# Kernel tuning notes

Hardware: AMD Instinct MI355X
Metric: run time of the kernel (lower is better)

The kernel has to match this reference:

```python
import jax, jax.numpy as jnp
import numpy as np

B, N, DIN, DOUT = 64, 128, 64, 64
EDGE_P = 0.05  # adjacency density


def setup_inputs() -> dict:
    key = jax.random.key(0)
    k1, k2, k3, k4 = jax.random.split(key, 4)
    # 2D tuple features: X[b, i, k, :] is the feature of tuple (i, k) in graph b
    X = jax.random.normal(k1, (B, N, N, DIN), dtype=jnp.float32)
    # sparse adjacency realized densely as 0/1 floats (PygHO 'DD' masked mode)
    A = (jax.random.uniform(k2, (B, N, N)) < EDGE_P).astype(jnp.float32)
    # tuplewise MLP (default mlp={} -> single Linear indim->outdim)
    W = (jax.random.normal(k3, (DIN, DOUT), dtype=jnp.float32) / np.sqrt(DIN)).astype(jnp.float32)
    b = jnp.zeros((DOUT,), dtype=jnp.float32)
    return {"X": X, "A": A, "W": W, "b": b}


def reference(X, A, W, b):
    # tuplewiseapply(MLP): dense linear on the last (feature) dim of every tuple
    tX = jnp.einsum('bikd,de->bike', X, W) + b          # [B, N, N, DOUT]
    # OpMessagePassingOnSubg2D, aggr='sum':
    # out[b, i, j, :] = sum_k tX[b, i, k, :] * A[b, k, j]
    out = jnp.einsum('bike,bkj->bije', tX, A)           # [B, N, N, DOUT]
    return out
```

## Files before the change

### kernel.cpp

```cpp
#include <hip/hip_runtime.h>

#define NGRAPH 64
#define NN 128
#define DI 64
#define DO 64

typedef __attribute__((ext_vector_type(8))) short short8;
typedef __attribute__((ext_vector_type(4))) short short4v;
typedef __attribute__((ext_vector_type(4))) float f32x4;

#define OFF_COLSUM (2u * 1024u * 1024u)
#define OFF_WTHI   (OFF_COLSUM + 32u * 1024u)
#define OFF_WTLO   (OFF_WTHI + 8u * 1024u)
#define WS_NEED    (OFF_WTLO + 8u * 1024u)

__device__ __forceinline__ unsigned short f2bf_rn(float f) {
    unsigned int u = __float_as_uint(f);
    u += 0x7FFFu + ((u >> 16) & 1u);
    return (unsigned short)(u >> 16);
}
__device__ __forceinline__ float bf2f(unsigned short h) {
    return __uint_as_float(((unsigned int)h) << 16);
}

__global__ __launch_bounds__(256) void prep_adj(const float* __restrict__ A,
                                                short* __restrict__ AT,
                                                float* __restrict__ colsum) {
    __shared__ float csp[2][NN];
    const int b  = blockIdx.x;
    const int j  = threadIdx.x & 127;
    const int kh = threadIdx.x >> 7;
    const float* Ab = A + (size_t)b * NN * NN;
    short* ATr = AT + (size_t)b * NN * NN + (size_t)j * NN + kh * 64;
    float s = 0.f;
    for (int kc = 0; kc < 8; ++kc) {
        short8 pk;
        #pragma unroll
        for (int u = 0; u < 8; ++u) {
            float a = Ab[(size_t)(kh * 64 + kc * 8 + u) * NN + j];
            s += a;
            pk[u] = (short)f2bf_rn(a);
        }
        *(short8*)(ATr + kc * 8) = pk;
    }
    csp[kh][j] = s;
    __syncthreads();
    if (kh == 0) colsum[b * NN + j] = csp[0][j] + csp[1][j];
}

__global__ void prep_w(const float* __restrict__ W,
                       short* __restrict__ WThi, short* __restrict__ WTlo) {
    const int t = threadIdx.x;
    for (int m = 0; m < 16; ++m) {
        int idx = m * 256 + t;
        int e = idx >> 6, d = idx & 63;
        float x = W[d * 64 + e];
        unsigned short h = f2bf_rn(x);
        unsigned short lo = f2bf_rn(x - bf2f(h));
        WThi[idx] = (short)h;
        WTlo[idx] = (short)lo;
    }
}

#define TSTR 136

__global__ __launch_bounds__(256, 3)
void ngnn_main(const float* __restrict__ X,
               const short* __restrict__ AT,
               const float* __restrict__ bias,
               const float* __restrict__ colsum,
               const short* __restrict__ WThi,
               const short* __restrict__ WTlo,
               float* __restrict__ out) {
    __shared__ short tXThi[DO][TSTR];
    __shared__ short tXTlo[DO][TSTR];

    const int tid = threadIdx.x;
    const int w   = tid >> 6;
    const int l   = tid & 63;
    const int lm  = l & 15;
    const int lg  = l >> 4;
    const int b   = blockIdx.x >> 7;

    const float* Xb = X + (size_t)blockIdx.x * (NN * DI);

    short8 wfh[4][2], wfl[4][2];
    #pragma unroll
    for (int nt = 0; nt < 4; ++nt)
        #pragma unroll
        for (int ks = 0; ks < 2; ++ks) {
            int off = (nt * 16 + lm) * DI + ks * 32 + lg * 8;
            wfh[nt][ks] = *(const short8*)(WThi + off);
            wfl[nt][ks] = *(const short8*)(WTlo + off);
        }

    #pragma unroll
    for (int mt = 0; mt < 2; ++mt) {
        const int krow = (w * 2 + mt) * 16 + lm;
        const float* xr = Xb + (size_t)krow * DI;
        short8 xh[2], xl[2];
        #pragma unroll
        for (int ks = 0; ks < 2; ++ks) {
            float4 a = ((const float4*)xr)[ks * 8 + lg * 2];
            float4 c4 = ((const float4*)xr)[ks * 8 + lg * 2 + 1];
            float v[8] = {a.x, a.y, a.z, a.w, c4.x, c4.y, c4.z, c4.w};
            #pragma unroll
            for (int u = 0; u < 8; ++u) {
                unsigned short h = f2bf_rn(v[u]);
                xh[ks][u] = (short)h;
                xl[ks][u] = (short)f2bf_rn(v[u] - bf2f(h));
            }
        }
        #pragma unroll
        for (int nt = 0; nt < 4; ++nt) {
            f32x4 c = {0.f, 0.f, 0.f, 0.f};
            #pragma unroll
            for (int ks = 0; ks < 2; ++ks) {
                c = __builtin_amdgcn_mfma_f32_16x16x32_bf16(xh[ks], wfh[nt][ks], c, 0, 0, 0);
                c = __builtin_amdgcn_mfma_f32_16x16x32_bf16(xh[ks], wfl[nt][ks], c, 0, 0, 0);
                c = __builtin_amdgcn_mfma_f32_16x16x32_bf16(xl[ks], wfh[nt][ks], c, 0, 0, 0);
            }
            const int e  = nt * 16 + lm;
            const int kb = (w * 2 + mt) * 16 + lg * 4;
            short4v h4, l4;
            #pragma unroll
            for (int r = 0; r < 4; ++r) {
                unsigned short h = f2bf_rn(c[r]);
                h4[r] = (short)h;
                l4[r] = (short)f2bf_rn(c[r] - bf2f(h));
            }
            *(short4v*)&tXThi[e][kb] = h4;
            *(short4v*)&tXTlo[e][kb] = l4;
        }
    }
    __syncthreads();

    const short* ATb = AT + (size_t)b * NN * NN;
    f32x4 acc[8];
    #pragma unroll
    for (int nt = 0; nt < 8; ++nt) acc[nt] = (f32x4){0.f, 0.f, 0.f, 0.f};

    #pragma unroll
    for (int ks = 0; ks < 4; ++ks) {
        short8 ah = *(const short8*)&tXThi[w * 16 + lm][ks * 32 + lg * 8];
        short8 al = *(const short8*)&tXTlo[w * 16 + lm][ks * 32 + lg * 8];
        #pragma unroll
        for (int nt = 0; nt < 8; ++nt) {
            short8 bf = *(const short8*)(ATb + (size_t)(nt * 16 + lm) * NN + ks * 32 + lg * 8);
            acc[nt] = __builtin_amdgcn_mfma_f32_16x16x32_bf16(ah, bf, acc[nt], 0, 0, 0);
            acc[nt] = __builtin_amdgcn_mfma_f32_16x16x32_bf16(al, bf, acc[nt], 0, 0, 0);
        }
    }

    const int e0 = w * 16 + lg * 4;
    const float4 bv = *(const float4*)(bias + e0);
    float* outb = out + (size_t)blockIdx.x * (NN * DO);
    #pragma unroll
    for (int nt = 0; nt < 8; ++nt) {
        const int j = nt * 16 + lm;
        const float cs = colsum[b * NN + j];
        float4 o;
        o.x = acc[nt][0] + bv.x * cs;
        o.y = acc[nt][1] + bv.y * cs;
        o.z = acc[nt][2] + bv.z * cs;
        o.w = acc[nt][3] + bv.w * cs;
        *(float4*)(outb + (size_t)j * DO + e0) = o;
    }
}

__global__ __launch_bounds__(256, 3)
void fallback_dense(const float* __restrict__ X,
                    const float* __restrict__ A,
                    const float* __restrict__ W,
                    const float* __restrict__ bias,
                    float* __restrict__ out) {
    __shared__ float tXs[NN][DO + 4];
    __shared__ float Ws[DI][DO];
    __shared__ float bs[DO];
    const int tid = threadIdx.x;
    const int bb = blockIdx.x >> 7;

    {
        const float4* Wv = (const float4*)W;
        float4* Wsv = (float4*)&Ws[0][0];
        #pragma unroll
        for (int t = 0; t < 4; ++t) Wsv[tid + 256 * t] = Wv[tid + 256 * t];
        if (tid < DO) bs[tid] = bias[tid];
    }
    __syncthreads();
    {
        const int k = tid & 127;
        const int e0 = (tid >> 7) * 32;
        const float4* Xv = (const float4*)(X + (size_t)blockIdx.x * (NN * DI) + (size_t)k * DI);
        float acc[32];
        #pragma unroll
        for (int q = 0; q < 32; ++q) acc[q] = 0.f;
        for (int dq = 0; dq < DI / 4; ++dq) {
            float4 xv = Xv[dq];
            const float xs[4] = {xv.x, xv.y, xv.z, xv.w};
            #pragma unroll
            for (int s = 0; s < 4; ++s) {
                const float4* wrow = (const float4*)&Ws[dq * 4 + s][e0];
                #pragma unroll
                for (int q = 0; q < 8; ++q) {
                    float4 wv = wrow[q];
                    acc[q * 4 + 0] = fmaf(xs[s], wv.x, acc[q * 4 + 0]);
                    acc[q * 4 + 1] = fmaf(xs[s], wv.y, acc[q * 4 + 1]);
                    acc[q * 4 + 2] = fmaf(xs[s], wv.z, acc[q * 4 + 2]);
                    acc[q * 4 + 3] = fmaf(xs[s], wv.w, acc[q * 4 + 3]);
                }
            }
        }
        float4* trow = (float4*)&tXs[k][e0];
        #pragma unroll
        for (int q = 0; q < 8; ++q)
            trow[q] = make_float4(acc[q * 4], acc[q * 4 + 1], acc[q * 4 + 2], acc[q * 4 + 3]);
    }
    __syncthreads();
    {
        const int lane = tid & 63;
        const int g = tid >> 6;
        const float bl = bs[lane];
        float* outb = out + (size_t)blockIdx.x * (NN * DO);
        for (int jj = 0; jj < 32; ++jj) {
            const int j = g * 32 + jj;
            const float* Acol = A + (size_t)bb * NN * NN + j;
            float acc2 = 0.f, cs = 0.f;
            for (int k = 0; k < NN; ++k) {
                float a = Acol[(size_t)k * NN];
                cs += a;
                acc2 = fmaf(a, tXs[k][lane], acc2);
            }
            outb[(size_t)j * DO + lane] = acc2 + bl * cs;
        }
    }
}

extern "C" void kernel_launch(void* const* d_in, const int* in_sizes, int n_in,
                              void* d_out, int out_size, void* d_ws, size_t ws_size,
                              hipStream_t stream) {
    const float* X    = (const float*)d_in[0];
    const float* A    = (const float*)d_in[1];
    const float* W    = (const float*)d_in[2];
    const float* bias = (const float*)d_in[3];
    float* out = (float*)d_out;

    if (d_ws != nullptr && ws_size >= WS_NEED) {
        char* ws = (char*)d_ws;
        short* ATp    = (short*)ws;
        float* colsum = (float*)(ws + OFF_COLSUM);
        short* WThi   = (short*)(ws + OFF_WTHI);
        short* WTlo   = (short*)(ws + OFF_WTLO);

        hipLaunchKernelGGL(prep_adj, dim3(NGRAPH), dim3(256), 0, stream, A, ATp, colsum);
        hipLaunchKernelGGL(prep_w, dim3(1), dim3(256), 0, stream, W, WThi, WTlo);
        hipLaunchKernelGGL(ngnn_main, dim3(NGRAPH * NN), dim3(256), 0, stream,
                           X, ATp, bias, colsum, WThi, WTlo, out);
    } else {
        hipLaunchKernelGGL(fallback_dense, dim3(NGRAPH * NN), dim3(256), 0, stream,
                           X, A, W, bias, out);
    }
}
```

Baseline: 570.8 us.

## Prefetch X, adjacency and colsum early; split prep_adj across more blocks

The main kernel now issues all global loads up front (raw X rows, the first adjacency slice, colsum values and bias) so their latency overlaps the first GEMM. W fragments are loaded per output tile rather than all held at once, and the occupancy hint rises from 3 to 4 blocks per CU. prep_adj is split into 4 blocks per graph with 8 k-slices each, giving it more parallelism. The cost is higher register pressure from the prefetched values, which could cause spilling at the tighter launch bound.

```diff
diff --git a/kernel.cpp b/kernel.cpp
--- a/kernel.cpp
+++ b/kernel.cpp
@@ -26,31 +26,40 @@
 __global__ __launch_bounds__(256) void prep_adj(const float* __restrict__ A,
                                                 short* __restrict__ AT,
                                                 float* __restrict__ colsum) {
-    __shared__ float csp[2][NN];
-    const int b  = blockIdx.x;
-    const int j  = threadIdx.x & 127;
-    const int kh = threadIdx.x >> 7;
+    const int b  = blockIdx.x >> 2;
+    const int jq = blockIdx.x & 3;
+    const int jl = threadIdx.x & 31;
+    const int j  = jq * 32 + jl;
+    const int k8 = threadIdx.x >> 5;
+    __shared__ float csp[8][32];
     const float* Ab = A + (size_t)b * NN * NN;
-    short* ATr = AT + (size_t)b * NN * NN + (size_t)j * NN + kh * 64;
+    short* ATr = AT + (size_t)b * NN * NN + (size_t)j * NN + k8 * 16;
     float s = 0.f;
-    for (int kc = 0; kc < 8; ++kc) {
+    #pragma unroll
+    for (int c = 0; c < 2; ++c) {
         short8 pk;
         #pragma unroll
         for (int u = 0; u < 8; ++u) {
-            float a = Ab[(size_t)(kh * 64 + kc * 8 + u) * NN + j];
+            float a = Ab[(size_t)(k8 * 16 + c * 8 + u) * NN + j];
             s += a;
             pk[u] = (short)f2bf_rn(a);
         }
-        *(short8*)(ATr + kc * 8) = pk;
-    }
-    csp[kh][j] = s;
-    __syncthreads();
-    if (kh == 0) colsum[b * NN + j] = csp[0][j] + csp[1][j];
+        *(short8*)(ATr + c * 8) = pk;
+    }
+    csp[k8][jl] = s;
+    __syncthreads();
+    if (k8 == 0) {
+        float t = 0.f;
+        #pragma unroll
+        for (int q = 0; q < 8; ++q) t += csp[q][jl];
+        colsum[b * NN + j] = t;
+    }
 }
 
 __global__ void prep_w(const float* __restrict__ W,
                        short* __restrict__ WThi, short* __restrict__ WTlo) {
     const int t = threadIdx.x;
+    #pragma unroll
     for (int m = 0; m < 16; ++m) {
         int idx = m * 256 + t;
         int e = idx >> 6, d = idx & 63;
@@ -64,7 +73,7 @@
 
 #define TSTR 136
 
-__global__ __launch_bounds__(256, 3)
+__global__ __launch_bounds__(256, 4)
 void ngnn_main(const float* __restrict__ X,
                const short* __restrict__ AT,
                const float* __restrict__ bias,
@@ -82,44 +91,61 @@
     const int lg  = l >> 4;
     const int b   = blockIdx.x >> 7;
 
-    const float* Xb = X + (size_t)blockIdx.x * (NN * DI);
-
-    short8 wfh[4][2], wfl[4][2];
-    #pragma unroll
-    for (int nt = 0; nt < 4; ++nt)
+    const float* Xb  = X + (size_t)blockIdx.x * (NN * DI);
+    const short* ATb = AT + (size_t)b * NN * NN;
+
+    const float4* xr0 = (const float4*)(Xb + (size_t)((w * 2 + 0) * 16 + lm) * DI);
+    const float4* xr1 = (const float4*)(Xb + (size_t)((w * 2 + 1) * 16 + lm) * DI);
+    float4 xraw[8];
+    #pragma unroll
+    for (int ks = 0; ks < 2; ++ks) {
+        xraw[ks * 2 + 0]     = xr0[ks * 8 + lg * 2];
+        xraw[ks * 2 + 1]     = xr0[ks * 8 + lg * 2 + 1];
+        xraw[4 + ks * 2 + 0] = xr1[ks * 8 + lg * 2];
+        xraw[4 + ks * 2 + 1] = xr1[ks * 8 + lg * 2 + 1];
+    }
+    short8 bf0[8];
+    #pragma unroll
+    for (int nt = 0; nt < 8; ++nt)
+        bf0[nt] = *(const short8*)(ATb + (size_t)(nt * 16 + lm) * NN + lg * 8);
+    float csv[8];
+    #pragma unroll
+    for (int nt = 0; nt < 8; ++nt)
+        csv[nt] = colsum[b * NN + nt * 16 + lm];
+    const float4 bv = *(const float4*)(bias + w * 16 + lg * 4);
+
+    short8 xh[2][2], xl[2][2];
+    #pragma unroll
+    for (int mt = 0; mt < 2; ++mt)
         #pragma unroll
         for (int ks = 0; ks < 2; ++ks) {
-            int off = (nt * 16 + lm) * DI + ks * 32 + lg * 8;
-            wfh[nt][ks] = *(const short8*)(WThi + off);
-            wfl[nt][ks] = *(const short8*)(WTlo + off);
-        }
-
-    #pragma unroll
-    for (int mt = 0; mt < 2; ++mt) {
-        const int krow = (w * 2 + mt) * 16 + lm;
-        const float* xr = Xb + (size_t)krow * DI;
-        short8 xh[2], xl[2];
-        #pragma unroll
-        for (int ks = 0; ks < 2; ++ks) {
-            float4 a = ((const float4*)xr)[ks * 8 + lg * 2];
-            float4 c4 = ((const float4*)xr)[ks * 8 + lg * 2 + 1];
+            float4 a  = xraw[mt * 4 + ks * 2];
+            float4 c4 = xraw[mt * 4 + ks * 2 + 1];
             float v[8] = {a.x, a.y, a.z, a.w, c4.x, c4.y, c4.z, c4.w};
             #pragma unroll
             for (int u = 0; u < 8; ++u) {
                 unsigned short h = f2bf_rn(v[u]);
-                xh[ks][u] = (short)h;
-                xl[ks][u] = (short)f2bf_rn(v[u] - bf2f(h));
-            }
-        }
-        #pragma unroll
-        for (int nt = 0; nt < 4; ++nt) {
+                xh[mt][ks][u] = (short)h;
+                xl[mt][ks][u] = (short)f2bf_rn(v[u] - bf2f(h));
+            }
+        }
+
+    const int eo = lm * DI + lg * 8;
+    #pragma unroll
+    for (int nt = 0; nt < 4; ++nt) {
+        const short8 wh0 = *(const short8*)(WThi + nt * 16 * DI + eo);
+        const short8 wh1 = *(const short8*)(WThi + nt * 16 * DI + eo + 32);
+        const short8 wl0 = *(const short8*)(WTlo + nt * 16 * DI + eo);
+        const short8 wl1 = *(const short8*)(WTlo + nt * 16 * DI + eo + 32);
+        #pragma unroll
+        for (int mt = 0; mt < 2; ++mt) {
             f32x4 c = {0.f, 0.f, 0.f, 0.f};
-            #pragma unroll
-            for (int ks = 0; ks < 2; ++ks) {
-                c = __builtin_amdgcn_mfma_f32_16x16x32_bf16(xh[ks], wfh[nt][ks], c, 0, 0, 0);
-                c = __builtin_amdgcn_mfma_f32_16x16x32_bf16(xh[ks], wfl[nt][ks], c, 0, 0, 0);
-                c = __builtin_amdgcn_mfma_f32_16x16x32_bf16(xl[ks], wfh[nt][ks], c, 0, 0, 0);
-            }
+            c = __builtin_amdgcn_mfma_f32_16x16x32_bf16(xh[mt][0], wh0, c, 0, 0, 0);
+            c = __builtin_amdgcn_mfma_f32_16x16x32_bf16(xh[mt][0], wl0, c, 0, 0, 0);
+            c = __builtin_amdgcn_mfma_f32_16x16x32_bf16(xl[mt][0], wh0, c, 0, 0, 0);
+            c = __builtin_amdgcn_mfma_f32_16x16x32_bf16(xh[mt][1], wh1, c, 0, 0, 0);
+            c = __builtin_amdgcn_mfma_f32_16x16x32_bf16(xh[mt][1], wl1, c, 0, 0, 0);
+            c = __builtin_amdgcn_mfma_f32_16x16x32_bf16(xl[mt][1], wh1, c, 0, 0, 0);
             const int e  = nt * 16 + lm;
             const int kb = (w * 2 + mt) * 16 + lg * 4;
             short4v h4, l4;
@@ -135,30 +161,36 @@
     }
     __syncthreads();
 
-    const short* ATb = AT + (size_t)b * NN * NN;
     f32x4 acc[8];
     #pragma unroll
     for (int nt = 0; nt < 8; ++nt) acc[nt] = (f32x4){0.f, 0.f, 0.f, 0.f};
 
     #pragma unroll
     for (int ks = 0; ks < 4; ++ks) {
-        short8 ah = *(const short8*)&tXThi[w * 16 + lm][ks * 32 + lg * 8];
-        short8 al = *(const short8*)&tXTlo[w * 16 + lm][ks * 32 + lg * 8];
+        const short8 ah = *(const short8*)&tXThi[w * 16 + lm][ks * 32 + lg * 8];
+        const short8 al = *(const short8*)&tXTlo[w * 16 + lm][ks * 32 + lg * 8];
+        short8 bfv[8];
+        if (ks == 0) {
+            #pragma unroll
+            for (int nt = 0; nt < 8; ++nt) bfv[nt] = bf0[nt];
+        } else {
+            #pragma unroll
+            for (int nt = 0; nt < 8; ++nt)
+                bfv[nt] = *(const short8*)(ATb + (size_t)(nt * 16 + lm) * NN + ks * 32 + lg * 8);
+        }
         #pragma unroll
         for (int nt = 0; nt < 8; ++nt) {
-            short8 bf = *(const short8*)(ATb + (size_t)(nt * 16 + lm) * NN + ks * 32 + lg * 8);
-            acc[nt] = __builtin_amdgcn_mfma_f32_16x16x32_bf16(ah, bf, acc[nt], 0, 0, 0);
-            acc[nt] = __builtin_amdgcn_mfma_f32_16x16x32_bf16(al, bf, acc[nt], 0, 0, 0);
+            acc[nt] = __builtin_amdgcn_mfma_f32_16x16x32_bf16(ah, bfv[nt], acc[nt], 0, 0, 0);
+            acc[nt] = __builtin_amdgcn_mfma_f32_16x16x32_bf16(al, bfv[nt], acc[nt], 0, 0, 0);
         }
     }
 
     const int e0 = w * 16 + lg * 4;
-    const float4 bv = *(const float4*)(bias + e0);
     float* outb = out + (size_t)blockIdx.x * (NN * DO);
     #pragma unroll
     for (int nt = 0; nt < 8; ++nt) {
         const int j = nt * 16 + lm;
-        const float cs = colsum[b * NN + j];
+        const float cs = csv[nt];
         float4 o;
         o.x = acc[nt][0] + bv.x * cs;
         o.y = acc[nt][1] + bv.y * cs;
@@ -179,7 +211,6 @@
     __shared__ float bs[DO];
     const int tid = threadIdx.x;
     const int bb = blockIdx.x >> 7;
-
     {
         const float4* Wv = (const float4*)W;
         float4* Wsv = (float4*)&Ws[0][0];
@@ -252,7 +283,7 @@
         short* WThi   = (short*)(ws + OFF_WTHI);
         short* WTlo   = (short*)(ws + OFF_WTLO);
 
-        hipLaunchKernelGGL(prep_adj, dim3(NGRAPH), dim3(256), 0, stream, A, ATp, colsum);
+        hipLaunchKernelGGL(prep_adj, dim3(NGRAPH * 4), dim3(256), 0, stream, A, ATp, colsum);
         hipLaunchKernelGGL(prep_w, dim3(1), dim3(256), 0, stream, W, WThi, WTlo);
         hipLaunchKernelGGL(ngnn_main, dim3(NGRAPH * NN), dim3(256), 0, stream,
                            X, ATp, bias, colsum, WThi, WTlo, out);
```

Result: slower. 598.1 us (+4.8%).
